# Optimization experiments

Hardware: AMD Instinct MI355X
Metric: run time of the kernel (lower is better)

Reference implementation:

```python
import jax, jax.numpy as jnp
import numpy as np

N, C, H, W = 32, 1, 100, 168
STRIDE = 8
PRE_NMS_TOP_N = 1000   # pre_nms_top_n
POST_NMS_TOP_N = 100   # fpn_post_nms_top_n
PRE_NMS_THRESH = 0.01  # hardcoded in original forward_for_single_feature_map
NMS_THRESH = 0.5
MIN_SIZE = 0


def setup_inputs() -> dict:
    key = jax.random.key(0)
    k1, k2, k3 = jax.random.split(key, 3)
    # FCOS location grid at stride 8, flattened in (H, W) row-major order to match
    # permute(0,2,3,1).reshape(N,-1,...) layout of the predictions.
    xs = jnp.arange(W, dtype=jnp.float32) * STRIDE + STRIDE // 2
    ys = jnp.arange(H, dtype=jnp.float32) * STRIDE + STRIDE // 2
    xg, yg = jnp.meshgrid(xs, ys)  # (H, W); xg[h,w]=xs[w], yg[h,w]=ys[h]
    locations = jnp.stack([xg.ravel(), yg.ravel()], axis=-1)  # [H*W, 2]
    box_cls = jax.random.normal(k1, (N, C, H, W), jnp.float32) * 2.0 - 2.0
    box_regression = jax.random.uniform(k2, (N, 4, H, W), jnp.float32) * 64.0
    centerness = jax.random.normal(k3, (N, 1, H, W), jnp.float32)
    return {"locations": locations, "box_cls": box_cls,
            "box_regression": box_regression, "centerness": centerness,
            "image_h": 800, "image_w": 1344}


def _pairwise_iou(boxes):
    # boxes: [K, 4] xyxy
    x1, y1, x2, y2 = boxes[:, 0], boxes[:, 1], boxes[:, 2], boxes[:, 3]
    area = jnp.maximum(x2 - x1, 0.0) * jnp.maximum(y2 - y1, 0.0)
    iw = jnp.maximum(jnp.minimum(x2[:, None], x2[None, :]) - jnp.maximum(x1[:, None], x1[None, :]), 0.0)
    ih = jnp.maximum(jnp.minimum(y2[:, None], y2[None, :]) - jnp.maximum(y1[:, None], y1[None, :]), 0.0)
    inter = iw * ih
    union = area[:, None] + area[None, :] - inter
    return inter / jnp.maximum(union, 1e-9)


def _nms_keep(iou, valid):
    # Greedy NMS on boxes already sorted by descending score. valid marks real
    # (above-threshold, non-small) candidates; invalid boxes never suppress.
    K = valid.shape[0]
    idx = jnp.arange(K)

    def body(keep, i):
        sup = jnp.take(keep, i) & (jnp.take(iou, i, axis=0) > NMS_THRESH) & (idx > i)
        return keep & ~sup, None

    keep, _ = jax.lax.scan(body, valid, idx)
    return keep


def _single_image(scores, reg, locations, img_h, img_w):
    # scores: [H*W*C] sigmoid probs (class-major last, idx%C=class, idx//C=loc)
    # reg:    [H*W, 4] (l, t, r, b) distances
    top_scores, top_idx = jax.lax.top_k(scores, PRE_NMS_TOP_N)  # sorted desc
    loc_idx = top_idx // C
    labels = (top_idx % C + 1).astype(jnp.float32)
    valid = top_scores > PRE_NMS_THRESH  # candidate_inds = box_cls > thresh
    locs = jnp.take(locations, loc_idx, axis=0)  # [K, 2]
    r = jnp.take(reg, loc_idx, axis=0)           # [K, 4]
    # box decode + clip_to_image (TO_REMOVE=1 convention of BoxList)
    x1 = jnp.clip(locs[:, 0] - r[:, 0], 0.0, img_w - 1.0)
    y1 = jnp.clip(locs[:, 1] - r[:, 1], 0.0, img_h - 1.0)
    x2 = jnp.clip(locs[:, 0] + r[:, 2], 0.0, img_w - 1.0)
    y2 = jnp.clip(locs[:, 1] + r[:, 3], 0.0, img_h - 1.0)
    # remove_small_boxes (ws/hs with TO_REMOVE=1)
    valid = valid & ((x2 - x1 + 1.0) >= MIN_SIZE) & ((y2 - y1 + 1.0) >= MIN_SIZE)
    boxes = jnp.stack([x1, y1, x2, y2], axis=1)  # [K, 4]
    keep = _nms_keep(_pairwise_iou(boxes), valid)  # single fg class -> one NMS
    kept_scores = jnp.where(keep, top_scores, 0.0)
    # keep top fpn_post_nms_top_n by score (kthvalue threshold equivalent)
    final_scores, fi = jax.lax.top_k(kept_scores, POST_NMS_TOP_N)
    det = jnp.concatenate([jnp.take(boxes, fi, axis=0),
                           final_scores[:, None],
                           jnp.take(labels, fi)[:, None]], axis=1)  # [K_out, 6]
    return det


def reference(locations, box_cls, box_regression, centerness, image_h, image_w):
    # [N,C,H,W] -> [N, H*W*C] sigmoid scores (matches permute+reshape+sigmoid)
    scores = jax.nn.sigmoid(jnp.transpose(box_cls, (0, 2, 3, 1)).reshape(N, -1))
    reg = jnp.transpose(box_regression, (0, 2, 3, 1)).reshape(N, -1, 4)
    _ = jax.nn.sigmoid(centerness.reshape(N, -1))  # computed by original, unused in scoring
    img_h = jnp.float32(image_h)
    img_w = jnp.float32(image_w)
    det = jax.vmap(lambda s, r: _single_image(s, r, locations, img_h, img_w))(scores, reg)
    return det  # [N, POST_NMS_TOP_N, 6] = (x1,y1,x2,y2,score,label); score==0 rows are padding
```

## Files before the change

### kernel.cpp

```cpp
#include <hip/hip_runtime.h>
#include <cstdint>


typedef unsigned long long u64;
typedef unsigned int u32;

#define HW_TOT 16800
#define W_GRID 168
#define K_PRE  1000
#define NRANK  1024
#define N_IMG  32

#define SCORES_OFF 0
#define VALID_OFF  (N_IMG * NRANK * 4)
#define BOXES_OFF  (VALID_OFF + N_IMG * NRANK * 4)
#define MASK_OFF   (BOXES_OFF + N_IMG * NRANK * 16)
#define WS_NEED    ((size_t)MASK_OFF + (size_t)N_IMG * NRANK * 16 * 8)

__global__ __launch_bounds__(1024) void fcos_topk(
    const float* __restrict__ box_cls, const float* __restrict__ box_reg,
    const int* __restrict__ imh, const int* __restrict__ imw,
    float* __restrict__ scores_ws, u32* __restrict__ valid_ws,
    float* __restrict__ boxes_ws)
{
  const int n = blockIdx.x;
  const int t = threadIdx.x;
  const int lane = t & 63;
  __shared__ u32 hist[256];
  __shared__ u64 prefix_s;
  __shared__ u32 kneed_s, cnt_s;
  __shared__ u64 skey[1024];

  u64 kreg[17];
  const float* cls = box_cls + (size_t)n * HW_TOT;
  #pragma unroll
  for (int k = 0; k < 17; ++k) {
    int i = t + k * 1024;
    u64 key = 0;
    if (i < HW_TOT) {
      float x = cls[i];
      double sd = 1.0 / (1.0 + exp(-(double)x));
      float s = (float)sd;
      u32 b = __float_as_uint(s);
      u32 u = (b & 0x80000000u) ? ~b : (b | 0x80000000u);
      key = ((u64)u << 16) | (u64)(0xFFFFu - (u32)i);
    }
    kreg[k] = key;
  }
  if (t == 0) { prefix_s = 0ull; kneed_s = K_PRE; cnt_s = 0u; }
  __syncthreads();

  for (int p = 5; p >= 0; --p) {
    if (t < 256) hist[t] = 0u;
    __syncthreads();
    const u64 pref = prefix_s;
    const int sh = p * 8;
    #pragma unroll
    for (int k = 0; k < 17; ++k) {
      u64 key = kreg[k];
      bool act = ((key >> (sh + 8)) == pref);
      u32 bin = (u32)((key >> sh) & 0xFFull);
      u64 same = __ballot(act);
      #pragma unroll
      for (int b = 0; b < 8; ++b) {
        u64 bb = __ballot(act && ((bin >> b) & 1u));
        same &= ((bin >> b) & 1u) ? bb : ~bb;
      }
      if (act) {
        int ldr = __ffsll((long long)same) - 1;
        if (lane == ldr) atomicAdd(&hist[bin], (u32)__popcll(same));
      }
    }
    __syncthreads();
    if (t < 64) {
      u32 h0 = hist[4*t], h1 = hist[4*t+1], h2 = hist[4*t+2], h3 = hist[4*t+3];
      u32 bs = h0 + h1 + h2 + h3, s = bs;
      #pragma unroll
      for (int off = 1; off < 64; off <<= 1) {
        u32 tmp = __shfl_down(s, off);
        if (t + off < 64) s += tmp;
      }
      u32 tail = s - bs;
      hist[4*t+3] = h3 + tail;
      hist[4*t+2] = h2 + h3 + tail;
      hist[4*t+1] = h1 + h2 + h3 + tail;
      hist[4*t]   = bs + tail;
    }
    __syncthreads();
    bool sel = false; u32 kn = 0, gt = 0;
    if (t < 256) {
      u32 ge = hist[t];
      gt = (t < 255) ? hist[t + 1] : 0u;
      kn = kneed_s;
      sel = (ge >= kn) && (gt < kn);
    }
    const u64 curp = prefix_s;
    __syncthreads();
    if (sel) { prefix_s = (curp << 8) | (u64)t; kneed_s = kn - gt; }
    __syncthreads();
  }

  const u64 T = prefix_s;
  skey[t] = 0ull;
  __syncthreads();
  #pragma unroll
  for (int k = 0; k < 17; ++k) {
    if (kreg[k] >= T) {
      u32 pos = atomicAdd(&cnt_s, 1u);
      if (pos < 1024u) skey[pos] = kreg[k];
    }
  }
  __syncthreads();

  u64 key = skey[t];
  #pragma unroll
  for (u32 k2 = 2; k2 <= 64; k2 <<= 1) {
    #pragma unroll
    for (u32 j = k2 >> 1; j > 0; j >>= 1) {
      u64 other = __shfl_xor(key, (int)j);
      bool takeMax = (((t & k2) == 0) == ((t & j) == 0));
      u64 mx = key > other ? key : other;
      u64 mn = key > other ? other : key;
      key = takeMax ? mx : mn;
    }
  }
  #pragma unroll
  for (u32 k2 = 128; k2 <= 1024; k2 <<= 1) {
    for (u32 j = k2 >> 1; j >= 64; j >>= 1) {
      skey[t] = key;
      __syncthreads();
      u64 other = skey[t ^ j];
      __syncthreads();
      bool takeMax = (((t & k2) == 0) == ((t & j) == 0));
      u64 mx = key > other ? key : other;
      u64 mn = key > other ? other : key;
      key = takeMax ? mx : mn;
    }
    #pragma unroll
    for (u32 j = 32; j > 0; j >>= 1) {
      u64 other = __shfl_xor(key, (int)j);
      bool takeMax = (((t & k2) == 0) == ((t & j) == 0));
      u64 mx = key > other ? key : other;
      u64 mn = key > other ? other : key;
      key = takeMax ? mx : mn;
    }
  }

  const float fw = (float)(*imw) - 1.0f;
  const float fh = (float)(*imh) - 1.0f;
  float* bx = boxes_ws + ((size_t)n * NRANK + t) * 4;
  if (t < K_PRE) {
    u32 u = (u32)(key >> 16);
    u32 b = (u & 0x80000000u) ? (u & 0x7FFFFFFFu) : ~u;
    float s = __uint_as_float(b);
    u32 idx = 0xFFFFu - (u32)(key & 0xFFFFull);
    int hh = (int)idx / W_GRID, ww = (int)idx - hh * W_GRID;
    float lx = (float)(ww * 8 + 4), ly = (float)(hh * 8 + 4);
    const float* rg = box_reg + (size_t)n * 4 * HW_TOT + idx;
    float r0 = rg[0], r1 = rg[HW_TOT], r2 = rg[2 * HW_TOT], r3 = rg[3 * HW_TOT];
    float x1 = fminf(fmaxf(lx - r0, 0.0f), fw);
    float y1 = fminf(fmaxf(ly - r1, 0.0f), fh);
    float x2 = fminf(fmaxf(lx + r2, 0.0f), fw);
    float y2 = fminf(fmaxf(ly + r3, 0.0f), fh);
    bool valid = (s > 0.01f) && ((x2 - x1 + 1.0f) >= 0.0f)
                             && ((y2 - y1 + 1.0f) >= 0.0f);
    scores_ws[n * NRANK + t] = s;
    valid_ws[n * NRANK + t] = valid ? 1u : 0u;
    bx[0] = x1; bx[1] = y1; bx[2] = x2; bx[3] = y2;
  } else {
    scores_ws[n * NRANK + t] = 0.0f;
    valid_ws[n * NRANK + t] = 0u;
    bx[0] = 0.0f; bx[1] = 0.0f; bx[2] = 0.0f; bx[3] = 0.0f;
  }
}

__global__ __launch_bounds__(1024) void fcos_mask(
    const float* __restrict__ boxes_ws, u64* __restrict__ mask_ws)
{
  const int n = blockIdx.y, g = blockIdx.x;
  const int t = threadIdx.x;
  __shared__ float4 bx[1024];
  bx[t] = ((const float4*)boxes_ws)[(size_t)n * NRANK + t];
  __syncthreads();
  const int wv = t >> 6, lane = t & 63;

  float4 bj[16]; float aj[16];
  #pragma unroll
  for (int c = 0; c < 16; ++c) {
    bj[c] = bx[c * 64 + lane];
    aj[c] = __fmul_rn(fmaxf(bj[c].z - bj[c].x, 0.0f), fmaxf(bj[c].w - bj[c].y, 0.0f));
  }

  u64* mimg = mask_ws + (size_t)n * NRANK * 16;
  for (int r = wv; r < 125; r += 16) {
    const int i = r * 8 + g;
    const float4 bi = bx[i];
    const float ai = __fmul_rn(fmaxf(bi.z - bi.x, 0.0f), fmaxf(bi.w - bi.y, 0.0f));
    const int cmax = i >> 6;
    #pragma unroll
    for (int c = 0; c < 16; ++c) {
      if (c <= cmax) {
        float iw  = fmaxf(fminf(bi.z, bj[c].z) - fmaxf(bi.x, bj[c].x), 0.0f);
        float ih2 = fmaxf(fminf(bi.w, bj[c].w) - fmaxf(bi.y, bj[c].y), 0.0f);
        float inter = __fmul_rn(iw, ih2);
        float uni = fmaxf(__fsub_rn(__fadd_rn(ai, aj[c]), inter), 1e-9f);
        float iou = inter / uni;
        u64 m = __ballot(iou > 0.5f);
        if (lane == 0) mimg[(size_t)i * 16 + c] = m;
      }
    }
  }
}

__global__ __launch_bounds__(64) void fcos_scan(
    const float* __restrict__ scores_ws, const u32* __restrict__ valid_ws,
    const float* __restrict__ boxes_ws, const u64* __restrict__ mask_ws,
    float* __restrict__ out)
{
  const int n = blockIdx.x;
  const int lane = threadIdx.x;
  const u64 lowm = (1ull << lane) - 1ull;
  const u64* mbase = mask_ws + (size_t)n * NRANK * 16;

  u64 vw[16];
  #pragma unroll
  for (int w = 0; w < 16; ++w)
    vw[w] = __ballot(valid_ws[n * NRANK + w * 64 + lane] != 0u);

  u64 keptw[16];
  #pragma unroll
  for (int w = 0; w < 16; ++w) keptw[w] = 0ull;

  ulonglong2 A2[8], B2[8];
#define WORD(ARR, w) ((w) & 1 ? ARR[(w) >> 1].y : ARR[(w) >> 1].x)
#define LOADBLK(DST, BLK) do { \
    const ulonglong2* _p = (const ulonglong2*)(mbase + (((size_t)(BLK)) * 64 + (size_t)lane) * 16); \
    _Pragma("unroll") \
    for (int _r = 0; _r < 8; ++_r) DST[_r] = _p[_r]; \
  } while (0)
#define PROCBLK(ARR, BV) do { \
    u64 _acc = 0ull; \
    _Pragma("unroll") \
    for (int _w = 0; _w < 16; ++_w) \
      if (_w < (BV)) _acc |= WORD(ARR, _w) & keptw[_w]; \
    u64 _live = vw[(BV)] & ~__ballot(_acc != 0ull); \
    const u64 _row = WORD(ARR, (BV)); \
    u64 _kb = 0ull; \
    while (_live) { \
      u64 _blk = __ballot((_row & _live & lowm) != 0ull); \
      u64 _S = _live & ~_blk; \
      _kb |= _S; \
      u64 _supS = __ballot((_row & _S & lowm) != 0ull); \
      _live &= ~(_S | _supS); \
    } \
    keptw[(BV)] = _kb; \
  } while (0)

  LOADBLK(A2, 0);
  LOADBLK(B2, 1);   PROCBLK(A2, 0);
  LOADBLK(A2, 2);   PROCBLK(B2, 1);
  LOADBLK(B2, 3);   PROCBLK(A2, 2);
  LOADBLK(A2, 4);   PROCBLK(B2, 3);
  LOADBLK(B2, 5);   PROCBLK(A2, 4);
  LOADBLK(A2, 6);   PROCBLK(B2, 5);
  LOADBLK(B2, 7);   PROCBLK(A2, 6);
  LOADBLK(A2, 8);   PROCBLK(B2, 7);
  LOADBLK(B2, 9);   PROCBLK(A2, 8);
  LOADBLK(A2, 10);  PROCBLK(B2, 9);
  LOADBLK(B2, 11);  PROCBLK(A2, 10);
  LOADBLK(A2, 12);  PROCBLK(B2, 11);
  LOADBLK(B2, 13);  PROCBLK(A2, 12);
  LOADBLK(A2, 14);  PROCBLK(B2, 13);
  LOADBLK(B2, 15);  PROCBLK(A2, 14);
                    PROCBLK(B2, 15);
#undef PROCBLK
#undef LOADBLK
#undef WORD

  __shared__ u64 kw_s[16];
  __shared__ u32 cumk_s[17], cumn_s[17];
  if (lane == 0) {
    #pragma unroll
    for (int w = 0; w < 16; ++w) kw_s[w] = keptw[w];
  }
  __syncthreads();
  if (lane == 0) {
    u32 ck = 0, cn = 0;
    for (int w = 0; w < 16; ++w) {
      cumk_s[w] = ck; cumn_s[w] = cn;
      u64 rm = (w == 15) ? ((1ull << 40) - 1ull) : ~0ull;
      ck += (u32)__popcll(kw_s[w] & rm);
      cn += (u32)__popcll(~kw_s[w] & rm);
    }
    cumk_s[16] = ck; cumn_s[16] = cn;
  }
  __syncthreads();
  const u32 mtot = cumk_s[16];

  for (int s = lane; s < 100; s += 64) {
    u32 r; float sc;
    if ((u32)s < mtot) {
      int w = 0;
      #pragma unroll
      for (int x = 1; x < 16; ++x) if (cumk_s[x] <= (u32)s) w = x;
      u64 rm = (w == 15) ? ((1ull << 40) - 1ull) : ~0ull;
      u64 word = kw_s[w] & rm;
      u32 b = (u32)s - cumk_s[w];
      for (u32 z = 0; z < b; ++z) word &= word - 1;
      r = (u32)(w * 64) + (u32)(__ffsll((long long)word) - 1);
      sc = scores_ws[n * NRANK + r];
    } else {
      u32 s2 = (u32)s - mtot;
      int w = 0;
      #pragma unroll
      for (int x = 1; x < 16; ++x) if (cumn_s[x] <= s2) w = x;
      u64 rm = (w == 15) ? ((1ull << 40) - 1ull) : ~0ull;
      u64 word = (~kw_s[w]) & rm;
      u32 b = s2 - cumn_s[w];
      for (u32 z = 0; z < b; ++z) word &= word - 1;
      r = (u32)(w * 64) + (u32)(__ffsll((long long)word) - 1);
      sc = 0.0f;
    }
    const float* bxp = boxes_ws + ((size_t)n * NRANK + r) * 4;
    float* o = out + ((size_t)n * 100 + s) * 6;
    o[0] = bxp[0]; o[1] = bxp[1]; o[2] = bxp[2]; o[3] = bxp[3];
    o[4] = sc; o[5] = 1.0f;
  }
}

extern "C" void kernel_launch(void* const* d_in, const int* in_sizes, int n_in,
                              void* d_out, int out_size, void* d_ws, size_t ws_size,
                              hipStream_t stream) {
  (void)in_sizes; (void)n_in; (void)out_size;
  if (ws_size < WS_NEED) return;

  const float* box_cls = (const float*)d_in[1];
  const float* box_reg = (const float*)d_in[2];
  const int* imh = (const int*)d_in[4];
  const int* imw = (const int*)d_in[5];

  char* ws = (char*)d_ws;
  float* scores_ws = (float*)(ws + SCORES_OFF);
  u32*   valid_ws  = (u32*)(ws + VALID_OFF);
  float* boxes_ws  = (float*)(ws + BOXES_OFF);
  u64*   mask_ws   = (u64*)(ws + MASK_OFF);
  float* out = (float*)d_out;

  fcos_topk<<<N_IMG, 1024, 0, stream>>>(box_cls, box_reg, imh, imw,
                                        scores_ws, valid_ws, boxes_ws);
  dim3 gB(8, N_IMG);
  fcos_mask<<<gB, 1024, 0, stream>>>(boxes_ws, mask_ws);
  fcos_scan<<<N_IMG, 64, 0, stream>>>(scores_ws, valid_ws, boxes_ws, mask_ws, out);
}
```

Measured before the change: 160.8 us.

## Split top-k into parallel key/histogram pass and selection kernel; simplify intra-block NMS

The sigmoid and key computation, which uses double-precision exp, plus the first radix histogram pass now run in a separate kernel spread over 8x32 blocks. Partial histograms are merged into a global histogram with atomics. The selection kernel reads the precomputed keys and histogram, starts radix refinement from the second digit, and skips the ballot work for wavefronts with no active keys. The intra-block NMS loop now keeps the lowest live candidate one at a time instead of resolving several per iteration. This adds two kernel launches and a workspace round trip.

```diff
diff --git a/kernel.cpp b/kernel.cpp
--- a/kernel.cpp
+++ b/kernel.cpp
@@ -15,10 +15,58 @@
 #define VALID_OFF  (N_IMG * NRANK * 4)
 #define BOXES_OFF  (VALID_OFF + N_IMG * NRANK * 4)
 #define MASK_OFF   (BOXES_OFF + N_IMG * NRANK * 16)
-#define WS_NEED    ((size_t)MASK_OFF + (size_t)N_IMG * NRANK * 16 * 8)
-
-__global__ __launch_bounds__(1024) void fcos_topk(
-    const float* __restrict__ box_cls, const float* __restrict__ box_reg,
+#define UARR_OFF   (MASK_OFF + N_IMG * NRANK * 16 * 8)
+#define GHIST_OFF  (UARR_OFF + N_IMG * HW_TOT * 4)
+#define WS_NEED    ((size_t)GHIST_OFF + (size_t)N_IMG * 256 * 4)
+
+__global__ __launch_bounds__(1024) void fcos_zero(u32* __restrict__ ghist) {
+  ghist[blockIdx.x * 1024 + threadIdx.x] = 0u;
+}
+
+__global__ __launch_bounds__(256) void fcos_keys(
+    const float* __restrict__ box_cls, u32* __restrict__ uarr,
+    u32* __restrict__ ghist)
+{
+  const int n = blockIdx.y, g = blockIdx.x;
+  const int t = threadIdx.x;
+  const int lane = t & 63;
+  __shared__ u32 hist[256];
+  hist[t] = 0u;
+  __syncthreads();
+  const int base = g * 2100;
+  const float* cls = box_cls + (size_t)n * HW_TOT;
+  #pragma unroll
+  for (int k = 0; k < 9; ++k) {
+    int i = base + k * 256 + t;
+    bool ok = (i < base + 2100);
+    u32 u = 0;
+    if (ok) {
+      float x = cls[i];
+      double sd = 1.0 / (1.0 + exp(-(double)x));
+      float s = (float)sd;
+      u32 b = __float_as_uint(s);
+      u = (b & 0x80000000u) ? ~b : (b | 0x80000000u);
+      uarr[(size_t)n * HW_TOT + i] = u;
+    }
+    u32 bin = u >> 24;
+    u64 same = __ballot(ok);
+    #pragma unroll
+    for (int b2 = 0; b2 < 8; ++b2) {
+      u64 bb = __ballot(ok && ((bin >> b2) & 1u));
+      same &= ((bin >> b2) & 1u) ? bb : ~bb;
+    }
+    if (ok) {
+      int ldr = __ffsll((long long)same) - 1;
+      if (lane == ldr) atomicAdd(&hist[bin], (u32)__popcll(same));
+    }
+  }
+  __syncthreads();
+  if (hist[t]) atomicAdd(&ghist[n * 256 + t], hist[t]);
+}
+
+__global__ __launch_bounds__(1024) void fcos_sel(
+    const u32* __restrict__ uarr, const u32* __restrict__ ghist,
+    const float* __restrict__ box_reg,
     const int* __restrict__ imh, const int* __restrict__ imw,
     float* __restrict__ scores_ws, u32* __restrict__ valid_ws,
     float* __restrict__ boxes_ws)
@@ -32,25 +80,46 @@
   __shared__ u64 skey[1024];
 
   u64 kreg[17];
-  const float* cls = box_cls + (size_t)n * HW_TOT;
+  const u32* uimg = uarr + (size_t)n * HW_TOT;
   #pragma unroll
   for (int k = 0; k < 17; ++k) {
     int i = t + k * 1024;
-    u64 key = 0;
-    if (i < HW_TOT) {
-      float x = cls[i];
-      double sd = 1.0 / (1.0 + exp(-(double)x));
-      float s = (float)sd;
-      u32 b = __float_as_uint(s);
-      u32 u = (b & 0x80000000u) ? ~b : (b | 0x80000000u);
-      key = ((u64)u << 16) | (u64)(0xFFFFu - (u32)i);
-    }
-    kreg[k] = key;
+    kreg[k] = (i < HW_TOT)
+        ? (((u64)uimg[i] << 16) | (u64)(0xFFFFu - (u32)i)) : 0ull;
   }
   if (t == 0) { prefix_s = 0ull; kneed_s = K_PRE; cnt_s = 0u; }
-  __syncthreads();
-
-  for (int p = 5; p >= 0; --p) {
+
+  if (t < 256) hist[t] = ghist[n * 256 + t];
+  __syncthreads();
+  {
+    if (t < 64) {
+      u32 h0 = hist[4*t], h1 = hist[4*t+1], h2 = hist[4*t+2], h3 = hist[4*t+3];
+      u32 bs = h0 + h1 + h2 + h3, s = bs;
+      #pragma unroll
+      for (int off = 1; off < 64; off <<= 1) {
+        u32 tmp = __shfl_down(s, off);
+        if (t + off < 64) s += tmp;
+      }
+      u32 tail = s - bs;
+      hist[4*t+3] = h3 + tail;
+      hist[4*t+2] = h2 + h3 + tail;
+      hist[4*t+1] = h1 + h2 + h3 + tail;
+      hist[4*t]   = bs + tail;
+    }
+    __syncthreads();
+    bool sel = false; u32 kn = 0, gt = 0;
+    if (t < 256) {
+      u32 ge = hist[t];
+      gt = (t < 255) ? hist[t + 1] : 0u;
+      kn = kneed_s;
+      sel = (ge >= kn) && (gt < kn);
+    }
+    __syncthreads();
+    if (sel) { prefix_s = (u64)t; kneed_s = kn - gt; }
+    __syncthreads();
+  }
+
+  for (int p = 4; p >= 0; --p) {
     if (t < 256) hist[t] = 0u;
     __syncthreads();
     const u64 pref = prefix_s;
@@ -59,16 +128,18 @@
     for (int k = 0; k < 17; ++k) {
       u64 key = kreg[k];
       bool act = ((key >> (sh + 8)) == pref);
-      u32 bin = (u32)((key >> sh) & 0xFFull);
-      u64 same = __ballot(act);
-      #pragma unroll
-      for (int b = 0; b < 8; ++b) {
-        u64 bb = __ballot(act && ((bin >> b) & 1u));
-        same &= ((bin >> b) & 1u) ? bb : ~bb;
-      }
-      if (act) {
-        int ldr = __ffsll((long long)same) - 1;
-        if (lane == ldr) atomicAdd(&hist[bin], (u32)__popcll(same));
+      if (__ballot(act) != 0ull) {
+        u32 bin = (u32)((key >> sh) & 0xFFull);
+        u64 same = __ballot(act);
+        #pragma unroll
+        for (int b = 0; b < 8; ++b) {
+          u64 bb = __ballot(act && ((bin >> b) & 1u));
+          same &= ((bin >> b) & 1u) ? bb : ~bb;
+        }
+        if (act) {
+          int ldr = __ffsll((long long)same) - 1;
+          if (lane == ldr) atomicAdd(&hist[bin], (u32)__popcll(same));
+        }
       }
     }
     __syncthreads();
@@ -219,7 +290,6 @@
 {
   const int n = blockIdx.x;
   const int lane = threadIdx.x;
-  const u64 lowm = (1ull << lane) - 1ull;
   const u64* mbase = mask_ws + (size_t)n * NRANK * 16;
 
   u64 vw[16];
@@ -244,14 +314,13 @@
     for (int _w = 0; _w < 16; ++_w) \
       if (_w < (BV)) _acc |= WORD(ARR, _w) & keptw[_w]; \
     u64 _live = vw[(BV)] & ~__ballot(_acc != 0ull); \
-    const u64 _row = WORD(ARR, (BV)); \
+    const u64 _intra = WORD(ARR, (BV)); \
     u64 _kb = 0ull; \
     while (_live) { \
-      u64 _blk = __ballot((_row & _live & lowm) != 0ull); \
-      u64 _S = _live & ~_blk; \
-      _kb |= _S; \
-      u64 _supS = __ballot((_row & _S & lowm) != 0ull); \
-      _live &= ~(_S | _supS); \
+      u32 _i = (u32)(__ffsll((long long)_live) - 1); \
+      _kb |= (1ull << _i); \
+      u64 _sup = __ballot(((_intra >> _i) & 1ull) != 0ull); \
+      _live &= ~(_sup | (1ull << _i)); \
     } \
     keptw[(BV)] = _kb; \
   } while (0)
@@ -344,10 +413,15 @@
   u32*   valid_ws  = (u32*)(ws + VALID_OFF);
   float* boxes_ws  = (float*)(ws + BOXES_OFF);
   u64*   mask_ws   = (u64*)(ws + MASK_OFF);
+  u32*   uarr_ws   = (u32*)(ws + UARR_OFF);
+  u32*   ghist_ws  = (u32*)(ws + GHIST_OFF);
   float* out = (float*)d_out;
 
-  fcos_topk<<<N_IMG, 1024, 0, stream>>>(box_cls, box_reg, imh, imw,
-                                        scores_ws, valid_ws, boxes_ws);
+  fcos_zero<<<8, 1024, 0, stream>>>(ghist_ws);
+  dim3 gK(8, N_IMG);
+  fcos_keys<<<gK, 256, 0, stream>>>(box_cls, uarr_ws, ghist_ws);
+  fcos_sel<<<N_IMG, 1024, 0, stream>>>(uarr_ws, ghist_ws, box_reg, imh, imw,
+                                       scores_ws, valid_ws, boxes_ws);
   dim3 gB(8, N_IMG);
   fcos_mask<<<gB, 1024, 0, stream>>>(boxes_ws, mask_ws);
   fcos_scan<<<N_IMG, 64, 0, stream>>>(scores_ws, valid_ws, boxes_ws, mask_ws, out);
```

Result: slower. 171.7 us (+6.8%).
